# Optimization experiments

Measured on AMD Instinct MI355X. Metric: run time of the kernel, lower is better.

Reference implementation:

```python
import jax, jax.numpy as jnp
import numpy as np
from jax import lax

B, T, D, H = 256, 1024, 128, 256

def setup_inputs() -> dict:
    key = jax.random.key(0)
    ks = jax.random.split(key, 12)
    s_gate = 1.0 / np.sqrt(D + H)
    s_head = 1.0 / np.sqrt(2 * H)
    return {
        "x": jax.random.normal(ks[0], (B, T, D), jnp.float32),
        "Wi": jax.random.uniform(ks[1], (H, D + H), jnp.float32, -s_gate, s_gate),
        "bi": jax.random.uniform(ks[2], (H,), jnp.float32, -s_gate, s_gate),
        "Wf": jax.random.uniform(ks[3], (H, D + H), jnp.float32, -s_gate, s_gate),
        "bf": jax.random.uniform(ks[4], (H,), jnp.float32, -s_gate, s_gate),
        "Wo": jax.random.uniform(ks[5], (H, D + H), jnp.float32, -s_gate, s_gate),
        "bo": jax.random.uniform(ks[6], (H,), jnp.float32, -s_gate, s_gate),
        "Wc": jax.random.uniform(ks[7], (H, D + H), jnp.float32, -s_gate, s_gate),
        "bc": jax.random.uniform(ks[8], (H,), jnp.float32, -s_gate, s_gate),
        "W2": jax.random.uniform(ks[9], (1, 2 * H), jnp.float32, -s_head, s_head),
        "b2": jax.random.uniform(ks[10], (1,), jnp.float32, -s_head, s_head),
    }

def reference(x, Wi, bi, Wf, bf, Wo, bo, Wc, bc, W2, b2):
    # x: [B, T, D] -> scan over time dim
    xs = jnp.transpose(x, (1, 0, 2))  # [T, B, D]
    b, h = xs.shape[1], Wi.shape[0]
    h0 = jnp.zeros((b, h), x.dtype)
    c0 = jnp.zeros((b, h), x.dtype)

    def step(carry, xt):
        hid, cov = carry
        comb = jnp.concatenate([xt, hid], axis=1)  # [B, D+H]
        i = jax.nn.sigmoid(comb @ Wi.T + bi)
        f = jax.nn.sigmoid(comb @ Wf.T + bf)
        o = jax.nn.sigmoid(comb @ Wo.T + bo)
        c_tilde = jnp.tanh(comb @ Wc.T + bc)
        cov = f * cov + i * c_tilde
        hid = o * jnp.tanh(cov)
        return (hid, cov), None

    (hid, cov), _ = lax.scan(step, (h0, c0), xs)
    out = jax.nn.sigmoid(jnp.concatenate([hid, cov], axis=1) @ W2.T + b2)  # [B, 1]
    return out, hid
```

## Files before the change

### kernel.cpp

```cpp
#include <hip/hip_runtime.h>
#include <hip/hip_fp16.h>


typedef _Float16 half8 __attribute__((ext_vector_type(8)));
typedef float f32x4 __attribute__((ext_vector_type(4)));

#define MFMA16(a, b, c) __builtin_amdgcn_mfma_f32_16x16x32_f16((a), (b), (c), 0, 0, 0)

__device__ __forceinline__ float2 h2f2(unsigned int u) {
  __half2 h;
  __builtin_memcpy(&h, &u, 4);
  return __half22float2(h);
}

__device__ __forceinline__ float lstm_elem(float a_i, float a_f, float a_o, float a_c,
                                           float& c) {
  float eA = __expf(-a_i);
  float eC = __expf(2.f * fminf(fmaxf(a_c, -15.f), 15.f));
  float ict = (eC - 1.f) * __builtin_amdgcn_rcpf((1.f + eA) * (eC + 1.f));
  float eF = __expf(-a_f);
  float fg = __builtin_amdgcn_rcpf(1.f + eF);
  float cv = fg * c + ict;
  c = cv;
  float eO = __expf(-a_o);
  float eV = __expf(2.f * fminf(fmaxf(cv, -15.f), 15.f));
  return (eV - 1.f) * __builtin_amdgcn_rcpf((1.f + eO) * (eV + 1.f));
}

__global__ void w16_kernel(const float* __restrict__ Wi, const float* __restrict__ Wf,
                           const float* __restrict__ Wo, const float* __restrict__ Wc,
                           __half* __restrict__ w16x)
{
  int g = blockIdx.x, c = threadIdx.x;
  int q = g >> 8;
  const float* Wq = (q == 0) ? Wi : (q == 1) ? Wf : (q == 2) ? Wo : Wc;
  w16x[g * 128 + c] = __float2half_rn(Wq[(size_t)(g & 255) * 384 + c]);
}

__global__ __launch_bounds__(256) void gx_kernel(
    const __half* __restrict__ w16x,
    const float* __restrict__ bi, const float* __restrict__ bf,
    const float* __restrict__ bo, const float* __restrict__ bc,
    const float* __restrict__ x, unsigned* __restrict__ gx, int t0)
{
  const int tid = threadIdx.x;
  const int l = tid & 63, wv = tid >> 6;
  const int kq = l >> 4, col = l & 15;
  const int tch = blockIdx.x, bg = blockIdx.y, gh = blockIdx.z;
  const size_t brow = (size_t)(bg * 16 + col);
  const int bg8 = bg * 2 + (kq >> 1);
  const int kqc = kq & 1;

#pragma unroll
  for (int mh = 0; mh < 2; ++mh) {
    half8 afr[4][4];
#pragma unroll
    for (int mm = 0; mm < 4; ++mm) {
      int tt = t0 + tch * 8 + mh * 4 + mm;
      const float* xp = x + (brow * 1024 + tt) * 128 + kq * 8;
#pragma unroll
      for (int k = 0; k < 4; ++k) {
        float4 a = *(const float4*)(xp + k * 32);
        float4 b = *(const float4*)(xp + k * 32 + 4);
        afr[mm][k] = {(_Float16)a.x, (_Float16)a.y, (_Float16)a.z, (_Float16)a.w,
                      (_Float16)b.x, (_Float16)b.y, (_Float16)b.z, (_Float16)b.w};
      }
    }
#pragma unroll
    for (int n = 0; n < 8; ++n) {
      int gbase = gh * 512 + wv * 128 + n * 16;
      int gcol = gbase + col;
      int q = gcol >> 8;
      const float* Bq = (q == 0) ? bi : (q == 1) ? bf : (q == 2) ? bo : bc;
      float bv = Bq[gcol & 255];
      half8 wf[4];
#pragma unroll
      for (int k = 0; k < 4; ++k)
        wf[k] = *(const half8*)(w16x + (size_t)(gbase + col) * 128 + k * 32 + kq * 8);
      int gt = gbase >> 4;
      int qg = gt >> 4;
      int wc = (gt & 15) >> 1, ctlc = gt & 1;
#pragma unroll
      for (int mm = 0; mm < 4; ++mm) {
        f32x4 acc = {bv, bv, bv, bv};
#pragma unroll
        for (int k = 0; k < 4; ++k) acc = MFMA16(afr[mm][k], wf[k], acc);
        int tl = tch * 8 + mh * 4 + mm;
        unsigned lo = (unsigned)__half_as_ushort(__float2half_rn(acc[0])) |
                      ((unsigned)__half_as_ushort(__float2half_rn(acc[1])) << 16);
        unsigned hi = (unsigned)__half_as_ushort(__float2half_rn(acc[2])) |
                      ((unsigned)__half_as_ushort(__float2half_rn(acc[3])) << 16);
        unsigned* gp = gx + (((((size_t)tl * 32 + bg8) * 8 + wc) * 4 + qg) * 16 + col) * 8 +
                       kqc * 4 + ctlc * 2;
        uint2 v = {lo, hi};
        *(uint2*)gp = v;
      }
    }
  }
}

#define NFV 46

#define WFRAG(ctl, q, kk)                                                     \
  ((((ctl) * 4 + (q)) * 8 + (kk)) < NFV                                       \
       ? wfr[(((ctl) * 4 + (q)) * 8 + (kk))]                                  \
       : *(const half8*)(WL + ((((ctl) * 4 + (q)) * 8 + (kk)) - NFV) * 1024 + lofs))

__global__ __launch_bounds__(512) __attribute__((amdgpu_waves_per_eu(2, 2)))
void rec_kernel(
    const float* __restrict__ Wi, const float* __restrict__ Wf,
    const float* __restrict__ Wo, const float* __restrict__ Wc,
    const unsigned* __restrict__ gx, float* __restrict__ dout,
    float* __restrict__ c_plain, float* __restrict__ c_state,
    __half* __restrict__ h_state, int t0, int tc)
{
  __shared__ char lds[163840];
  const int tid = threadIdx.x;
  const int l = tid & 63, w = tid >> 6;
  const int kq = l >> 4, col = l & 15;
  const int kqc = kq & 1;
  const int ctl_own = l >> 5;
  const int lofs = l * 16;
  const int bg8 = blockIdx.x;
  char* WL = lds + w * 18432;
  char* HF = lds + 147456;
  const int j2 = (w * 2 + ctl_own) * 16 + col;

  half8 wfr[NFV];
#pragma unroll
  for (int ctl = 0; ctl < 2; ++ctl) {
#pragma unroll
    for (int q = 0; q < 4; ++q) {
      const float* Wq = (q == 0) ? Wi : (q == 1) ? Wf : (q == 2) ? Wo : Wc;
      int j = (w * 2 + ctl) * 16 + col;
      const float* src = Wq + (size_t)j * 384 + 128 + kq * 8;
#pragma unroll
      for (int kk = 0; kk < 8; ++kk) {
        float4 a = *(const float4*)(src + kk * 32);
        float4 b = *(const float4*)(src + kk * 32 + 4);
        half8 h = {(_Float16)a.x, (_Float16)a.y, (_Float16)a.z, (_Float16)a.w,
                   (_Float16)b.x, (_Float16)b.y, (_Float16)b.z, (_Float16)b.w};
        int i = (ctl * 4 + q) * 8 + kk;
        if (i < NFV)
          wfr[i] = h;
        else
          *(half8*)(WL + (i - NFV) * 1024 + lofs) = h;
      }
    }
  }

  {
    uint4 z = {0, 0, 0, 0};
    *(uint4*)(HF + (tid >> 8) * 8192 + 4096 + (tid & 255) * 16) = z;
  }
  float cst[4];
  if (t0 == 0) {
#pragma unroll
    for (int i = 0; i < 4; ++i) cst[i] = 0.f;
    uint2 z2 = {0, 0};
    *(uint2*)(HF + tid * 8) = z2;
  } else {
#pragma unroll
    for (int rg = 0; rg < 4; ++rg)
      cst[rg] = c_state[(size_t)bg8 * 2048 + (kqc * 4 + rg) * 256 + j2];
    int r8 = tid >> 6, c4 = tid & 63;
    uint2 v = *(const uint2*)(h_state + (size_t)bg8 * 2048 + r8 * 256 + c4 * 4);
    *(uint2*)(HF + ((t0 & 1) << 13) + r8 * 512 + ((c4 * 8) ^ ((r8 & 7) << 4))) = v;
  }
  __syncthreads();

  const char* gxb = (const char*)gx + ((size_t)bg8 * 8 + w) * 2048 +
                    col * 32 + kqc * 16 + ctl_own * 8;
  uint2 gxv[4];
#pragma unroll
  for (int q = 0; q < 4; ++q) gxv[q] = *(const uint2*)(gxb + q * 512);

  const int rswz = (l & 7) << 4;
  const int rbase = (l & 15) * 512;
  const int baddr = (l & 31) * 4;

  for (int tt = 0; tt < tc; ++tt) {
    const int s = t0 + tt;
    const char* rb = HF + ((s & 1) << 13);
    char* wb = HF + (((s & 1) ^ 1) << 13);
    __syncthreads();

    const char* gxn = gxb + (size_t)((tt + 1 < tc) ? tt + 1 : tt) * 524288;
    uint2 gnv[4];
#pragma unroll
    for (int q = 0; q < 4; ++q) gnv[q] = *(const uint2*)(gxn + q * 512);

    f32x4 acc[2][4] = {{{0.f, 0.f, 0.f, 0.f}, {0.f, 0.f, 0.f, 0.f},
                        {0.f, 0.f, 0.f, 0.f}, {0.f, 0.f, 0.f, 0.f}},
                       {{0.f, 0.f, 0.f, 0.f}, {0.f, 0.f, 0.f, 0.f},
                        {0.f, 0.f, 0.f, 0.f}, {0.f, 0.f, 0.f, 0.f}}};
#pragma unroll
    for (int kk = 0; kk < 8; ++kk) {
      half8 afr = *(const half8*)(rb + rbase + ((kk * 64 + kq * 16) ^ rswz));
      acc[0][0] = MFMA16(afr, WFRAG(0, 0, kk), acc[0][0]);
      acc[0][1] = MFMA16(afr, WFRAG(0, 1, kk), acc[0][1]);
      acc[0][2] = MFMA16(afr, WFRAG(0, 2, kk), acc[0][2]);
      acc[0][3] = MFMA16(afr, WFRAG(0, 3, kk), acc[0][3]);
      acc[1][0] = MFMA16(afr, WFRAG(1, 0, kk), acc[1][0]);
      acc[1][1] = MFMA16(afr, WFRAG(1, 1, kk), acc[1][1]);
      acc[1][2] = MFMA16(afr, WFRAG(1, 2, kk), acc[1][2]);
      acc[1][3] = MFMA16(afr, WFRAG(1, 3, kk), acc[1][3]);
    }

    float P[4][4];
#pragma unroll
    for (int q = 0; q < 4; ++q) {
      auto pk01 = __builtin_amdgcn_cvt_pkrtz(acc[1][q][0], acc[1][q][1]);
      auto pk23 = __builtin_amdgcn_cvt_pkrtz(acc[1][q][2], acc[1][q][3]);
      int b01, b23;
      __builtin_memcpy(&b01, &pk01, 4);
      __builtin_memcpy(&b23, &pk23, 4);
      b01 = __builtin_amdgcn_ds_bpermute(baddr, b01);
      b23 = __builtin_amdgcn_ds_bpermute(baddr, b23);
      float2 u01 = h2f2((unsigned)b01);
      float2 u23 = h2f2((unsigned)b23);
      P[q][0] = ctl_own ? u01.x : acc[0][q][0];
      P[q][1] = ctl_own ? u01.y : acc[0][q][1];
      P[q][2] = ctl_own ? u23.x : acc[0][q][2];
      P[q][3] = ctl_own ? u23.y : acc[0][q][3];
    }

    const bool lastT = (s == 1023);
    const bool endC = (tt + 1 == tc);
    float g[4][4];
#pragma unroll
    for (int q = 0; q < 4; ++q) {
      float2 a = h2f2(gxv[q].x), b = h2f2(gxv[q].y);
      g[q][0] = a.x; g[q][1] = a.y; g[q][2] = b.x; g[q][3] = b.y;
    }
#pragma unroll
    for (int rg = 0; rg < 4; ++rg) {
      float hv = lstm_elem(P[0][rg] + g[0][rg], P[1][rg] + g[1][rg],
                           P[2][rg] + g[2][rg], P[3][rg] + g[3][rg], cst[rg]);
      int row = kqc * 4 + rg;
      *(_Float16*)(wb + row * 512 + ((j2 * 2) ^ ((row & 7) << 4))) = (_Float16)hv;
      if (lastT) {
        int rrow = bg8 * 8 + row;
        dout[256 + (size_t)rrow * 256 + j2] = hv;
        c_plain[(size_t)rrow * 256 + j2] = cst[rg];
      } else if (endC) {
        h_state[(size_t)bg8 * 2048 + row * 256 + j2] = __float2half_rn(hv);
      }
    }
#pragma unroll
    for (int q = 0; q < 4; ++q) gxv[q] = gnv[q];
  }

#pragma unroll
  for (int rg = 0; rg < 4; ++rg)
    c_state[(size_t)bg8 * 2048 + (kqc * 4 + rg) * 256 + j2] = cst[rg];
}

__global__ void head_kernel(const float* __restrict__ hid, const float* __restrict__ cpl,
                            const float* __restrict__ W2, const float* __restrict__ b2,
                            float* __restrict__ out)
{
  int b = blockIdx.x, l = threadIdx.x;
  float4 hv = ((const float4*)(hid + (size_t)b * 256))[l];
  float4 wv = ((const float4*)W2)[l];
  float s = hv.x * wv.x + hv.y * wv.y + hv.z * wv.z + hv.w * wv.w;
  float4 cv = ((const float4*)(cpl + (size_t)b * 256))[l];
  float4 wc = ((const float4*)(W2 + 256))[l];
  s += cv.x * wc.x + cv.y * wc.y + cv.z * wc.z + cv.w * wc.w;
#pragma unroll
  for (int off = 32; off > 0; off >>= 1) s += __shfl_down(s, off, 64);
  if (l == 0) out[b] = 1.f / (1.f + __expf(-(s + b2[0])));
}

extern "C" void kernel_launch(void* const* d_in, const int* in_sizes, int n_in,
                              void* d_out, int out_size, void* d_ws, size_t ws_size,
                              hipStream_t stream)
{
  const float* x  = (const float*)d_in[0];
  const float* Wi = (const float*)d_in[1];
  const float* bi = (const float*)d_in[2];
  const float* Wf = (const float*)d_in[3];
  const float* bf = (const float*)d_in[4];
  const float* Wo = (const float*)d_in[5];
  const float* bo = (const float*)d_in[6];
  const float* Wc = (const float*)d_in[7];
  const float* bc = (const float*)d_in[8];
  const float* W2 = (const float*)d_in[9];
  const float* b2 = (const float*)d_in[10];
  float* out = (float*)d_out;

  char* ws = (char*)d_ws;
  const size_t state_bytes = (size_t)896 * 1024;
  size_t avail = ws_size > state_bytes ? ws_size - state_bytes : 0;
  size_t tcap = avail / 524288;
  int TC = (int)(tcap > 1024 ? 1024 : (tcap & ~(size_t)7));
  if (TC < 8) TC = 8;
  unsigned* gxb = (unsigned*)ws;
  float* c_plain = (float*)(ws + (size_t)TC * 524288);
  float* c_state = c_plain + 65536;
  __half* h_state = (__half*)(c_state + 65536);
  __half* w16x = (__half*)(h_state + 65536);

  w16_kernel<<<1024, 128, 0, stream>>>(Wi, Wf, Wo, Wc, w16x);
  for (int t0 = 0; t0 < 1024; t0 += TC) {
    int tcn = (1024 - t0 < TC) ? (1024 - t0) : TC;
    gx_kernel<<<dim3(tcn / 8, 16, 2), 256, 0, stream>>>(w16x, bi, bf, bo, bc, x, gxb, t0);
    rec_kernel<<<32, 512, 0, stream>>>(Wi, Wf, Wo, Wc, gxb, out, c_plain, c_state,
                                       h_state, t0, tcn);
  }
  head_kernel<<<256, 64, 0, stream>>>(out + 256, c_plain, W2, b2, out);
}
```

Measured before the change: 3.108 ms.

## Fuse input projection into recurrent kernel with flag-based producer/consumer overlap

The separate gx_kernel launch is removed. Its input-projection GEMM now runs in extra blocks of one fused launch, alongside the 32 recurrent blocks. Producer blocks bump per-64-step chunk counters with release atomics, and recurrent blocks spin on those counters before consuming each chunk. This lets the recurrence start on early timesteps while later gate inputs are still being computed, instead of serializing the two kernels. It relies on the producer blocks actually being scheduled while the recurrent blocks spin, and the large LDS allocation per producer block could limit co-residency.

```diff
diff --git a/kernel.cpp b/kernel.cpp
--- a/kernel.cpp
+++ b/kernel.cpp
@@ -29,74 +29,13 @@
 
 __global__ void w16_kernel(const float* __restrict__ Wi, const float* __restrict__ Wf,
                            const float* __restrict__ Wo, const float* __restrict__ Wc,
-                           __half* __restrict__ w16x)
+                           __half* __restrict__ w16x, unsigned* __restrict__ flags)
 {
   int g = blockIdx.x, c = threadIdx.x;
+  if (g == 0 && c < 16) flags[c] = 0;
   int q = g >> 8;
   const float* Wq = (q == 0) ? Wi : (q == 1) ? Wf : (q == 2) ? Wo : Wc;
   w16x[g * 128 + c] = __float2half_rn(Wq[(size_t)(g & 255) * 384 + c]);
-}
-
-__global__ __launch_bounds__(256) void gx_kernel(
-    const __half* __restrict__ w16x,
-    const float* __restrict__ bi, const float* __restrict__ bf,
-    const float* __restrict__ bo, const float* __restrict__ bc,
-    const float* __restrict__ x, unsigned* __restrict__ gx, int t0)
-{
-  const int tid = threadIdx.x;
-  const int l = tid & 63, wv = tid >> 6;
-  const int kq = l >> 4, col = l & 15;
-  const int tch = blockIdx.x, bg = blockIdx.y, gh = blockIdx.z;
-  const size_t brow = (size_t)(bg * 16 + col);
-  const int bg8 = bg * 2 + (kq >> 1);
-  const int kqc = kq & 1;
-
-#pragma unroll
-  for (int mh = 0; mh < 2; ++mh) {
-    half8 afr[4][4];
-#pragma unroll
-    for (int mm = 0; mm < 4; ++mm) {
-      int tt = t0 + tch * 8 + mh * 4 + mm;
-      const float* xp = x + (brow * 1024 + tt) * 128 + kq * 8;
-#pragma unroll
-      for (int k = 0; k < 4; ++k) {
-        float4 a = *(const float4*)(xp + k * 32);
-        float4 b = *(const float4*)(xp + k * 32 + 4);
-        afr[mm][k] = {(_Float16)a.x, (_Float16)a.y, (_Float16)a.z, (_Float16)a.w,
-                      (_Float16)b.x, (_Float16)b.y, (_Float16)b.z, (_Float16)b.w};
-      }
-    }
-#pragma unroll
-    for (int n = 0; n < 8; ++n) {
-      int gbase = gh * 512 + wv * 128 + n * 16;
-      int gcol = gbase + col;
-      int q = gcol >> 8;
-      const float* Bq = (q == 0) ? bi : (q == 1) ? bf : (q == 2) ? bo : bc;
-      float bv = Bq[gcol & 255];
-      half8 wf[4];
-#pragma unroll
-      for (int k = 0; k < 4; ++k)
-        wf[k] = *(const half8*)(w16x + (size_t)(gbase + col) * 128 + k * 32 + kq * 8);
-      int gt = gbase >> 4;
-      int qg = gt >> 4;
-      int wc = (gt & 15) >> 1, ctlc = gt & 1;
-#pragma unroll
-      for (int mm = 0; mm < 4; ++mm) {
-        f32x4 acc = {bv, bv, bv, bv};
-#pragma unroll
-        for (int k = 0; k < 4; ++k) acc = MFMA16(afr[mm][k], wf[k], acc);
-        int tl = tch * 8 + mh * 4 + mm;
-        unsigned lo = (unsigned)__half_as_ushort(__float2half_rn(acc[0])) |
-                      ((unsigned)__half_as_ushort(__float2half_rn(acc[1])) << 16);
-        unsigned hi = (unsigned)__half_as_ushort(__float2half_rn(acc[2])) |
-                      ((unsigned)__half_as_ushort(__float2half_rn(acc[3])) << 16);
-        unsigned* gp = gx + (((((size_t)tl * 32 + bg8) * 8 + wc) * 4 + qg) * 16 + col) * 8 +
-                       kqc * 4 + ctlc * 2;
-        uint2 v = {lo, hi};
-        *(uint2*)gp = v;
-      }
-    }
-  }
 }
 
 #define NFV 46
@@ -107,17 +46,88 @@
        : *(const half8*)(WL + ((((ctl) * 4 + (q)) * 8 + (kk)) - NFV) * 1024 + lofs))
 
 __global__ __launch_bounds__(512) __attribute__((amdgpu_waves_per_eu(2, 2)))
-void rec_kernel(
+void fused_kernel(
     const float* __restrict__ Wi, const float* __restrict__ Wf,
     const float* __restrict__ Wo, const float* __restrict__ Wc,
-    const unsigned* __restrict__ gx, float* __restrict__ dout,
-    float* __restrict__ c_plain, float* __restrict__ c_state,
-    __half* __restrict__ h_state, int t0, int tc)
+    const __half* __restrict__ w16x,
+    const float* __restrict__ bi, const float* __restrict__ bf,
+    const float* __restrict__ bo, const float* __restrict__ bc,
+    const float* __restrict__ x, unsigned* __restrict__ gx,
+    float* __restrict__ dout, float* __restrict__ c_plain,
+    float* __restrict__ c_state, __half* __restrict__ h_state,
+    unsigned* __restrict__ flags, int t0, int tc)
 {
   __shared__ char lds[163840];
   const int tid = threadIdx.x;
-  const int l = tid & 63, w = tid >> 6;
+  const int l = tid & 63;
   const int kq = l >> 4, col = l & 15;
+
+  if (blockIdx.x >= 32) {
+    const int pid = (int)blockIdx.x - 32;
+    const int cch = pid >> 7, r = pid & 127;
+    const int tch = cch * 8 + (r & 7);
+    const int bg = r >> 3;
+    const int w8 = tid >> 6;
+    const int gh = w8 >> 2, wv = w8 & 3;
+    const size_t brow = (size_t)(bg * 16 + col);
+    const int bg8 = bg * 2 + (kq >> 1);
+    const int kqc = kq & 1;
+
+#pragma unroll
+    for (int mh = 0; mh < 2; ++mh) {
+      half8 afr[4][4];
+#pragma unroll
+      for (int mm = 0; mm < 4; ++mm) {
+        int tt = t0 + tch * 8 + mh * 4 + mm;
+        const float* xp = x + (brow * 1024 + tt) * 128 + kq * 8;
+#pragma unroll
+        for (int k = 0; k < 4; ++k) {
+          float4 a = *(const float4*)(xp + k * 32);
+          float4 b = *(const float4*)(xp + k * 32 + 4);
+          afr[mm][k] = {(_Float16)a.x, (_Float16)a.y, (_Float16)a.z, (_Float16)a.w,
+                        (_Float16)b.x, (_Float16)b.y, (_Float16)b.z, (_Float16)b.w};
+        }
+      }
+#pragma unroll
+      for (int n = 0; n < 8; ++n) {
+        int gbase = gh * 512 + wv * 128 + n * 16;
+        int gcol = gbase + col;
+        int q = gcol >> 8;
+        const float* Bq = (q == 0) ? bi : (q == 1) ? bf : (q == 2) ? bo : bc;
+        float bv = Bq[gcol & 255];
+        half8 wf[4];
+#pragma unroll
+        for (int k = 0; k < 4; ++k)
+          wf[k] = *(const half8*)(w16x + (size_t)(gbase + col) * 128 + k * 32 + kq * 8);
+        int gt = gbase >> 4;
+        int qg = gt >> 4;
+        int wc = (gt & 15) >> 1, ctlc = gt & 1;
+#pragma unroll
+        for (int mm = 0; mm < 4; ++mm) {
+          f32x4 acc = {bv, bv, bv, bv};
+#pragma unroll
+          for (int k = 0; k < 4; ++k) acc = MFMA16(afr[mm][k], wf[k], acc);
+          int tl = tch * 8 + mh * 4 + mm;
+          unsigned lo = (unsigned)__half_as_ushort(__float2half_rn(acc[0])) |
+                        ((unsigned)__half_as_ushort(__float2half_rn(acc[1])) << 16);
+          unsigned hi = (unsigned)__half_as_ushort(__float2half_rn(acc[2])) |
+                        ((unsigned)__half_as_ushort(__float2half_rn(acc[3])) << 16);
+          unsigned* gp = gx + (((((size_t)tl * 32 + bg8) * 8 + wc) * 4 + qg) * 16 + col) * 8 +
+                         kqc * 4 + ctlc * 2;
+          uint2 v = {lo, hi};
+          *(uint2*)gp = v;
+        }
+      }
+    }
+    __threadfence();
+    __syncthreads();
+    if (tid == 0)
+      __hip_atomic_fetch_add(&flags[(t0 >> 6) + cch], 1u, __ATOMIC_RELEASE,
+                             __HIP_MEMORY_SCOPE_AGENT);
+    return;
+  }
+
+  const int w = tid >> 6;
   const int kqc = kq & 1;
   const int ctl_own = l >> 5;
   const int lofs = l * 16;
@@ -171,9 +181,7 @@
 
   const char* gxb = (const char*)gx + ((size_t)bg8 * 8 + w) * 2048 +
                     col * 32 + kqc * 16 + ctl_own * 8;
-  uint2 gxv[4];
-#pragma unroll
-  for (int q = 0; q < 4; ++q) gxv[q] = *(const uint2*)(gxb + q * 512);
+  uint2 gxv[4] = {{0, 0}, {0, 0}, {0, 0}, {0, 0}};
 
   const int rswz = (l & 7) << 4;
   const int rbase = (l & 15) * 512;
@@ -183,6 +191,18 @@
     const int s = t0 + tt;
     const char* rb = HF + ((s & 1) << 13);
     char* wb = HF + (((s & 1) ^ 1) << 13);
+
+    if ((tt & 63) == 0) {
+      const int gci = s >> 6;
+      while (__hip_atomic_load(&flags[gci], __ATOMIC_RELAXED,
+                               __HIP_MEMORY_SCOPE_AGENT) < 128u) {
+        __builtin_amdgcn_s_sleep(1);
+      }
+      __builtin_amdgcn_fence(__ATOMIC_ACQUIRE, "agent");
+#pragma unroll
+      for (int q = 0; q < 4; ++q)
+        gxv[q] = *(const uint2*)(gxb + (size_t)tt * 524288 + q * 512);
+    }
     __syncthreads();
 
     const char* gxn = gxb + (size_t)((tt + 1 < tc) ? tt + 1 : tt) * 524288;
@@ -290,23 +310,24 @@
   float* out = (float*)d_out;
 
   char* ws = (char*)d_ws;
-  const size_t state_bytes = (size_t)896 * 1024;
+  const size_t state_bytes = (size_t)1024 * 1024;
   size_t avail = ws_size > state_bytes ? ws_size - state_bytes : 0;
   size_t tcap = avail / 524288;
-  int TC = (int)(tcap > 1024 ? 1024 : (tcap & ~(size_t)7));
-  if (TC < 8) TC = 8;
+  int TC = (int)(tcap > 1024 ? 1024 : (tcap & ~(size_t)63));
+  if (TC < 64) TC = 64;
   unsigned* gxb = (unsigned*)ws;
   float* c_plain = (float*)(ws + (size_t)TC * 524288);
   float* c_state = c_plain + 65536;
   __half* h_state = (__half*)(c_state + 65536);
   __half* w16x = (__half*)(h_state + 65536);
-
-  w16_kernel<<<1024, 128, 0, stream>>>(Wi, Wf, Wo, Wc, w16x);
+  unsigned* flags = (unsigned*)(w16x + 131072);
+
+  w16_kernel<<<1024, 128, 0, stream>>>(Wi, Wf, Wo, Wc, w16x, flags);
   for (int t0 = 0; t0 < 1024; t0 += TC) {
     int tcn = (1024 - t0 < TC) ? (1024 - t0) : TC;
-    gx_kernel<<<dim3(tcn / 8, 16, 2), 256, 0, stream>>>(w16x, bi, bf, bo, bc, x, gxb, t0);
-    rec_kernel<<<32, 512, 0, stream>>>(Wi, Wf, Wo, Wc, gxb, out, c_plain, c_state,
-                                       h_state, t0, tcn);
+    fused_kernel<<<32 + tcn * 2, 512, 0, stream>>>(
+        Wi, Wf, Wo, Wc, w16x, bi, bf, bo, bc, x, gxb, out, c_plain, c_state,
+        h_state, flags, t0, tcn);
   }
   head_kernel<<<256, 64, 0, stream>>>(out + 256, c_plain, W2, b2, out);
 }
```

Measured after the change: 3.529 ms. 13.6% more time.
